# Kernel tuning notes

Hardware: AMD Instinct MI355X
Metric: run time of the kernel (lower is better)

## Reference

```python
import jax, jax.numpy as jnp
import numpy as np

# Multi-level feature-map spatial shapes (compile-time constants, as in Deformable DETR
# for an 800x1333 input with strides 8/16/32/64).
SPATIAL_SHAPES = ((100, 167), (50, 84), (25, 42), (13, 21))
NUM_KEYS = sum(h * w for h, w in SPATIAL_SHAPES)  # 22223


def setup_inputs() -> dict:
    key = jax.random.key(0)
    k1, k2, k3 = jax.random.split(key, 3)
    bs, nq, nh, d, nl, npt = 8, 900, 8, 32, 4, 4
    value = jax.random.normal(k1, (bs, NUM_KEYS, nh, d), jnp.float32)
    sampling_locations = jax.random.uniform(k2, (bs, nq, nh, nl, npt, 2), jnp.float32)
    aw = jax.random.uniform(k3, (bs, nq, nh, nl, npt), jnp.float32)
    # module applies softmax over (levels*points) before calling the kernel
    aw = jax.nn.softmax(aw.reshape(bs, nq, nh, nl * npt), axis=-1).reshape(bs, nq, nh, nl, npt)
    return {"value": value, "sampling_locations": sampling_locations, "attention_weights": aw}


def _bilinear_sample(v_flat, H, W, x, y):
    # v_flat: (bs, nh, H*W, d); x, y: (bs, nh, P) pixel coords (align_corners=False convention)
    x0 = jnp.floor(x)
    y0 = jnp.floor(y)
    x1 = x0 + 1.0
    y1 = y0 + 1.0
    wx1 = x - x0
    wx0 = 1.0 - wx1
    wy1 = y - y0
    wy0 = 1.0 - wy1

    def gather(xi, yi):
        # zero padding: out-of-bounds corners contribute 0 (grid_sample padding_mode='zeros')
        valid = (xi >= 0) & (xi <= W - 1) & (yi >= 0) & (yi <= H - 1)
        xc = jnp.clip(xi, 0, W - 1).astype(jnp.int32)
        yc = jnp.clip(yi, 0, H - 1).astype(jnp.int32)
        idx = yc * W + xc  # (bs, nh, P)
        s = jnp.take_along_axis(v_flat, idx[..., None], axis=2)  # (bs, nh, P, d)
        return jnp.where(valid[..., None], s, jnp.zeros((), v_flat.dtype))

    return (gather(x0, y0) * (wx0 * wy0)[..., None]
            + gather(x1, y0) * (wx1 * wy0)[..., None]
            + gather(x0, y1) * (wx0 * wy1)[..., None]
            + gather(x1, y1) * (wx1 * wy1)[..., None])


def reference(value, sampling_locations, attention_weights):
    # value: (bs, num_keys, nh, d)
    # sampling_locations: (bs, nq, nh, nl, npt, 2), normalized (x, y) in [0, 1]
    # attention_weights: (bs, nq, nh, nl, npt)
    bs, _, nh, d = value.shape
    _, nq, _, nl, npt, _ = sampling_locations.shape
    out = jnp.zeros((bs, nh, nq, d), value.dtype)
    start = 0
    for lvl, (H, W) in enumerate(SPATIAL_SHAPES):
        v = value[:, start:start + H * W]                     # (bs, H*W, nh, d)
        start += H * W
        v = jnp.transpose(v, (0, 2, 1, 3))                    # (bs, nh, H*W, d)
        loc = sampling_locations[:, :, :, lvl]                # (bs, nq, nh, npt, 2)
        # grid = 2*loc - 1; pixel coord (align_corners=False): (g+1)*S/2 - 0.5 = loc*S - 0.5
        x = loc[..., 0] * W - 0.5
        y = loc[..., 1] * H - 0.5
        x = jnp.transpose(x, (0, 2, 1, 3)).reshape(bs, nh, nq * npt)
        y = jnp.transpose(y, (0, 2, 1, 3)).reshape(bs, nh, nq * npt)
        sampled = _bilinear_sample(v, H, W, x, y).reshape(bs, nh, nq, npt, d)
        w = jnp.transpose(attention_weights[:, :, :, lvl], (0, 2, 1, 3))  # (bs, nh, nq, npt)
        out = out + jnp.einsum('bhqpd,bhqp->bhqd', sampled, w)
    # torch output is (bs, nq, nh*d) with head-major channel layout
    return jnp.transpose(out, (0, 2, 1, 3)).reshape(bs, nq, nh * d)
```

## Files before the change

kernel.cpp:

```cpp
#include <hip/hip_runtime.h>


#define BS 8
#define NQ 900
#define NH 8
#define DD 32
#define NL 4
#define NPT 4
#define NUM_KEYS 22223

__global__ __launch_bounds__(256) void msda_kernel(
    const float* __restrict__ value,
    const float* __restrict__ loc,
    const float* __restrict__ aw,
    float* __restrict__ out)
{
    const int tid = blockIdx.x * blockDim.x + threadIdx.x;
    const int cg = tid & 7;
    const int h  = (tid >> 3) & 7;
    const int bq = tid >> 6;
    const int b  = bq / NQ;

    const int Hs[NL]  = {100, 50, 25, 13};
    const int Ws[NL]  = {167, 84, 42, 21};
    const int Sts[NL] = {0, 16700, 20900, 21950};

    const float4* __restrict__ v4 = (const float4*)value;
    const unsigned vbase = (unsigned)b * (NUM_KEYS * NH * 8) + h * 8 + cg;

    const float2* __restrict__ loc2 = (const float2*)loc;
    const int lbase = (bq * NH + h) * (NL * NPT);

    float4 acc = {0.f, 0.f, 0.f, 0.f};

    #pragma unroll
    for (int lvl = 0; lvl < NL; ++lvl) {
        const int H = Hs[lvl], W = Ws[lvl];
        const unsigned lvbase = vbase + (unsigned)Sts[lvl] * (NH * 8);
        const unsigned rowstride = (unsigned)W * (NH * 8);

        #pragma unroll
        for (int p = 0; p < NPT; ++p) {
            const int li = lbase + lvl * NPT + p;
            const float2 xy = loc2[li];
            const float w  = aw[li];

            const float x = xy.x * (float)W - 0.5f;
            const float y = xy.y * (float)H - 0.5f;
            const float fx0 = floorf(x);
            const float fy0 = floorf(y);
            const int x0 = (int)fx0;
            const int y0 = (int)fy0;
            float wx1 = x - fx0, wy1 = y - fy0;
            float wx0 = 1.f - wx1, wy0 = 1.f - wy1;

            wx0 = (x0 >= 0 && x0 <= W - 1)     ? wx0 : 0.f;
            wx1 = (x0 + 1 >= 0 && x0 + 1 <= W - 1) ? wx1 : 0.f;
            wy0 = (y0 >= 0 && y0 <= H - 1)     ? wy0 : 0.f;
            wy1 = (y0 + 1 >= 0 && y0 + 1 <= H - 1) ? wy1 : 0.f;

            const int x0c = min(max(x0, 0), W - 1);
            const int x1c = min(max(x0 + 1, 0), W - 1);
            const int y0c = min(max(y0, 0), H - 1);
            const int y1c = min(max(y0 + 1, 0), H - 1);

            const unsigned r0 = lvbase + (unsigned)y0c * rowstride;
            const unsigned r1 = lvbase + (unsigned)y1c * rowstride;

            const float4 v00 = v4[r0 + (unsigned)x0c * (NH * 8)];
            const float4 v01 = v4[r0 + (unsigned)x1c * (NH * 8)];
            const float4 v10 = v4[r1 + (unsigned)x0c * (NH * 8)];
            const float4 v11 = v4[r1 + (unsigned)x1c * (NH * 8)];

            const float s00 = w * wx0 * wy0;
            const float s01 = w * wx1 * wy0;
            const float s10 = w * wx0 * wy1;
            const float s11 = w * wx1 * wy1;

            acc.x = fmaf(s00, v00.x, acc.x); acc.y = fmaf(s00, v00.y, acc.y);
            acc.z = fmaf(s00, v00.z, acc.z); acc.w = fmaf(s00, v00.w, acc.w);
            acc.x = fmaf(s01, v01.x, acc.x); acc.y = fmaf(s01, v01.y, acc.y);
            acc.z = fmaf(s01, v01.z, acc.z); acc.w = fmaf(s01, v01.w, acc.w);
            acc.x = fmaf(s10, v10.x, acc.x); acc.y = fmaf(s10, v10.y, acc.y);
            acc.z = fmaf(s10, v10.z, acc.z); acc.w = fmaf(s10, v10.w, acc.w);
            acc.x = fmaf(s11, v11.x, acc.x); acc.y = fmaf(s11, v11.y, acc.y);
            acc.z = fmaf(s11, v11.z, acc.z); acc.w = fmaf(s11, v11.w, acc.w);
        }
    }

    float4* __restrict__ out4 = (float4*)out;
    out4[(bq * NH + h) * 8 + cg] = acc;
}

extern "C" void kernel_launch(void* const* d_in, const int* in_sizes, int n_in,
                              void* d_out, int out_size, void* d_ws, size_t ws_size,
                              hipStream_t stream) {
    const float* value = (const float*)d_in[0];
    const float* loc   = (const float*)d_in[1];
    const float* aw    = (const float*)d_in[2];
    float* out = (float*)d_out;

    const int total = BS * NQ * NH * 8;
    const int block = 256;
    const int grid = total / block;
    msda_kernel<<<grid, block, 0, stream>>>(value, loc, aw, out);
}
```

Before: 260.2 us.

## Split levels across lanes and reduce partial sums with wavefront shuffles

Each thread now handles one feature level instead of looping over all four, which gives four times as many threads. The level partial sums are combined with xor-shuffles across lanes 8 and 16 inside the wavefront, and only the level-0 lanes write the output. Location and weight loads become float4 vector loads per (query, head, level). This exposes more memory-level parallelism for the gather-bound work, at the cost of redundant index math and extra shuffle instructions.

```diff
diff --git a/kernel.cpp b/kernel.cpp
--- a/kernel.cpp
+++ b/kernel.cpp
@@ -4,7 +4,6 @@
 #define BS 8
 #define NQ 900
 #define NH 8
-#define DD 32
 #define NL 4
 #define NPT 4
 #define NUM_KEYS 22223
@@ -15,81 +14,90 @@
     const float* __restrict__ aw,
     float* __restrict__ out)
 {
-    const int tid = blockIdx.x * blockDim.x + threadIdx.x;
-    const int cg = tid & 7;
-    const int h  = (tid >> 3) & 7;
-    const int bq = tid >> 6;
-    const int b  = bq / NQ;
+    const int tid = blockIdx.x * 256 + threadIdx.x;
+    const int cg  = tid & 7;
+    const int lvl = (tid >> 3) & 3;
+    const int h   = (tid >> 5) & 7;
+    const int bq  = tid >> 8;
+    const int b   = bq / NQ;
 
-    const int Hs[NL]  = {100, 50, 25, 13};
-    const int Ws[NL]  = {167, 84, 42, 21};
-    const int Sts[NL] = {0, 16700, 20900, 21950};
+    const bool l01 = lvl < 2;
+    const int H  = l01 ? (lvl == 0 ? 100 : 50)    : (lvl == 2 ? 25 : 13);
+    const int W  = l01 ? (lvl == 0 ? 167 : 84)    : (lvl == 2 ? 42 : 21);
+    const int St = l01 ? (lvl == 0 ? 0 : 16700)   : (lvl == 2 ? 20900 : 21950);
 
     const float4* __restrict__ v4 = (const float4*)value;
-    const unsigned vbase = (unsigned)b * (NUM_KEYS * NH * 8) + h * 8 + cg;
+    const unsigned vbase = (unsigned)b * (NUM_KEYS * NH * 8) + h * 8 + cg
+                         + (unsigned)St * (NH * 8);
+    const unsigned rowstride = (unsigned)W * (NH * 8);
 
-    const float2* __restrict__ loc2 = (const float2*)loc;
-    const int lbase = (bq * NH + h) * (NL * NPT);
+    const int lidx = (bq * NH + h) * NL + lvl;
+    const float4* __restrict__ loc4 = (const float4*)loc;
+    const float4* __restrict__ aw4  = (const float4*)aw;
+    const float4 xy01 = loc4[lidx * 2];
+    const float4 xy23 = loc4[lidx * 2 + 1];
+    const float4 wv   = aw4[lidx];
+
+    const float xs[NPT] = {xy01.x, xy01.z, xy23.x, xy23.z};
+    const float ys[NPT] = {xy01.y, xy01.w, xy23.y, xy23.w};
+    const float ws[NPT] = {wv.x, wv.y, wv.z, wv.w};
 
     float4 acc = {0.f, 0.f, 0.f, 0.f};
 
     #pragma unroll
-    for (int lvl = 0; lvl < NL; ++lvl) {
-        const int H = Hs[lvl], W = Ws[lvl];
-        const unsigned lvbase = vbase + (unsigned)Sts[lvl] * (NH * 8);
-        const unsigned rowstride = (unsigned)W * (NH * 8);
+    for (int p = 0; p < NPT; ++p) {
+        const float x = xs[p] * (float)W - 0.5f;
+        const float y = ys[p] * (float)H - 0.5f;
+        const float w = ws[p];
+        const float fx0 = floorf(x);
+        const float fy0 = floorf(y);
+        const int x0 = (int)fx0;
+        const int y0 = (int)fy0;
+        float wx1 = x - fx0, wy1 = y - fy0;
+        float wx0 = 1.f - wx1, wy0 = 1.f - wy1;
 
-        #pragma unroll
-        for (int p = 0; p < NPT; ++p) {
-            const int li = lbase + lvl * NPT + p;
-            const float2 xy = loc2[li];
-            const float w  = aw[li];
+        wx0 = (x0 >= 0 && x0 <= W - 1)         ? wx0 : 0.f;
+        wx1 = (x0 + 1 >= 0 && x0 + 1 <= W - 1) ? wx1 : 0.f;
+        wy0 = (y0 >= 0 && y0 <= H - 1)         ? wy0 : 0.f;
+        wy1 = (y0 + 1 >= 0 && y0 + 1 <= H - 1) ? wy1 : 0.f;
 
-            const float x = xy.x * (float)W - 0.5f;
-            const float y = xy.y * (float)H - 0.5f;
-            const float fx0 = floorf(x);
-            const float fy0 = floorf(y);
-            const int x0 = (int)fx0;
-            const int y0 = (int)fy0;
-            float wx1 = x - fx0, wy1 = y - fy0;
-            float wx0 = 1.f - wx1, wy0 = 1.f - wy1;
+        const int x0c = min(max(x0, 0), W - 1);
+        const int x1c = min(max(x0 + 1, 0), W - 1);
+        const int y0c = min(max(y0, 0), H - 1);
+        const int y1c = min(max(y0 + 1, 0), H - 1);
 
-            wx0 = (x0 >= 0 && x0 <= W - 1)     ? wx0 : 0.f;
-            wx1 = (x0 + 1 >= 0 && x0 + 1 <= W - 1) ? wx1 : 0.f;
-            wy0 = (y0 >= 0 && y0 <= H - 1)     ? wy0 : 0.f;
-            wy1 = (y0 + 1 >= 0 && y0 + 1 <= H - 1) ? wy1 : 0.f;
+        const unsigned r0 = vbase + (unsigned)y0c * rowstride;
+        const unsigned r1 = vbase + (unsigned)y1c * rowstride;
 
-            const int x0c = min(max(x0, 0), W - 1);
-            const int x1c = min(max(x0 + 1, 0), W - 1);
-            const int y0c = min(max(y0, 0), H - 1);
-            const int y1c = min(max(y0 + 1, 0), H - 1);
+        const float4 v00 = v4[r0 + (unsigned)x0c * (NH * 8)];
+        const float4 v01 = v4[r0 + (unsigned)x1c * (NH * 8)];
+        const float4 v10 = v4[r1 + (unsigned)x0c * (NH * 8)];
+        const float4 v11 = v4[r1 + (unsigned)x1c * (NH * 8)];
 
-            const unsigned r0 = lvbase + (unsigned)y0c * rowstride;
-            const unsigned r1 = lvbase + (unsigned)y1c * rowstride;
+        const float s00 = w * wx0 * wy0;
+        const float s01 = w * wx1 * wy0;
+        const float s10 = w * wx0 * wy1;
+        const float s11 = w * wx1 * wy1;
 
-            const float4 v00 = v4[r0 + (unsigned)x0c * (NH * 8)];
-            const float4 v01 = v4[r0 + (unsigned)x1c * (NH * 8)];
-            const float4 v10 = v4[r1 + (unsigned)x0c * (NH * 8)];
-            const float4 v11 = v4[r1 + (unsigned)x1c * (NH * 8)];
-
-            const float s00 = w * wx0 * wy0;
-            const float s01 = w * wx1 * wy0;
-            const float s10 = w * wx0 * wy1;
-            const float s11 = w * wx1 * wy1;
-
-            acc.x = fmaf(s00, v00.x, acc.x); acc.y = fmaf(s00, v00.y, acc.y);
-            acc.z = fmaf(s00, v00.z, acc.z); acc.w = fmaf(s00, v00.w, acc.w);
-            acc.x = fmaf(s01, v01.x, acc.x); acc.y = fmaf(s01, v01.y, acc.y);
-            acc.z = fmaf(s01, v01.z, acc.z); acc.w = fmaf(s01, v01.w, acc.w);
-            acc.x = fmaf(s10, v10.x, acc.x); acc.y = fmaf(s10, v10.y, acc.y);
-            acc.z = fmaf(s10, v10.z, acc.z); acc.w = fmaf(s10, v10.w, acc.w);
-            acc.x = fmaf(s11, v11.x, acc.x); acc.y = fmaf(s11, v11.y, acc.y);
-            acc.z = fmaf(s11, v11.z, acc.z); acc.w = fmaf(s11, v11.w, acc.w);
-        }
+        acc.x = fmaf(s00, v00.x, acc.x); acc.y = fmaf(s00, v00.y, acc.y);
+        acc.z = fmaf(s00, v00.z, acc.z); acc.w = fmaf(s00, v00.w, acc.w);
+        acc.x = fmaf(s01, v01.x, acc.x); acc.y = fmaf(s01, v01.y, acc.y);
+        acc.z = fmaf(s01, v01.z, acc.z); acc.w = fmaf(s01, v01.w, acc.w);
+        acc.x = fmaf(s10, v10.x, acc.x); acc.y = fmaf(s10, v10.y, acc.y);
+        acc.z = fmaf(s10, v10.z, acc.z); acc.w = fmaf(s10, v10.w, acc.w);
+        acc.x = fmaf(s11, v11.x, acc.x); acc.y = fmaf(s11, v11.y, acc.y);
+        acc.z = fmaf(s11, v11.z, acc.z); acc.w = fmaf(s11, v11.w, acc.w);
     }
 
-    float4* __restrict__ out4 = (float4*)out;
-    out4[(bq * NH + h) * 8 + cg] = acc;
+    acc.x += __shfl_xor(acc.x, 8);  acc.y += __shfl_xor(acc.y, 8);
+    acc.z += __shfl_xor(acc.z, 8);  acc.w += __shfl_xor(acc.w, 8);
+    acc.x += __shfl_xor(acc.x, 16); acc.y += __shfl_xor(acc.y, 16);
+    acc.z += __shfl_xor(acc.z, 16); acc.w += __shfl_xor(acc.w, 16);
+
+    if (lvl == 0) {
+        float4* __restrict__ out4 = (float4*)out;
+        out4[(bq * NH + h) * 8 + cg] = acc;
+    }
 }
 
 extern "C" void kernel_launch(void* const* d_in, const int* in_sizes, int n_in,
@@ -98,10 +106,10 @@
     const float* value = (const float*)d_in[0];
     const float* loc   = (const float*)d_in[1];
     const float* aw    = (const float*)d_in[2];
-    float* out = (float*)d_out;
+    float* outp = (float*)d_out;
 
-    const int total = BS * NQ * NH * 8;
+    const int total = BS * NQ * NH * NL * 8;
     const int block = 256;
     const int grid = total / block;
-    msda_kernel<<<grid, block, 0, stream>>>(value, loc, aw, out);
+    msda_kernel<<<grid, block, 0, stream>>>(value, loc, aw, outp);
 }
```

After: 254.2 us, median of 2. 2.3% less time.
